# Kernel tuning notes

Measured on AMD Instinct MI355X. Metric: run time of the kernel, lower is better.

## Reference

```python
import jax, jax.numpy as jnp
import numpy as np

LN_EPS = 1e-3  # keras LayerNormalization default epsilon

def setup_inputs() -> dict:
    key = jax.random.key(0)
    ks = jax.random.split(key, 8)
    B, T, N, F_in, F_out, S = 4, 4, 65536, 16, 32, 8
    E = 589824  # ~9 edges per node (8-neighbor grid + self loop)
    return {
        "water": jax.random.normal(ks[0], (B, T, N, F_in), jnp.float32),
        "static": jax.random.uniform(ks[1], (B, T, N, S), jnp.float32),
        "adj_rows": jax.random.randint(ks[2], (E,), 0, N, jnp.int32),
        "adj_cols": jax.random.randint(ks[3], (E,), 0, N, jnp.int32),
        "adj_vals": jax.random.uniform(ks[4], (E,), jnp.float32),
        "W_feat": (jax.random.normal(ks[5], (F_in, F_out), jnp.float32) * 0.1),
        "b_feat": jnp.zeros((F_out,), jnp.float32),
        "Wg1": (jax.random.normal(ks[6], (3, 1), jnp.float32) * 0.1),
        "bg1": jnp.zeros((1,), jnp.float32),
        "Wg2": (jax.random.normal(ks[7], (S - 3, 1), jnp.float32) * 0.1),
        "bg2": jnp.zeros((1,), jnp.float32),
        "ln_gamma": jnp.ones((F_out,), jnp.float32),
        "ln_beta": jnp.zeros((F_out,), jnp.float32),
        "min_gate": jnp.float32(0.1),
    }


def reference(water, static, adj_rows, adj_cols, adj_vals,
              W_feat, b_feat, Wg1, bg1, Wg2, bg2, ln_gamma, ln_beta, min_gate):
    B, T, N, F_in = water.shape
    # gated feature scaling: gate in (0,1], per (b,t,n)
    gate = jax.nn.sigmoid(static[..., :3] @ Wg1 + bg1) * jax.nn.sigmoid(static[..., 3:] @ Wg2 + bg2)
    gate = jnp.maximum(gate, min_gate)  # [B,T,N,1]
    x = (water * gate).reshape(B * T, N, F_in)
    # SpMM shared across all F_in channels and all B*T slices:
    # out[bt,n,f] = sum_{edges (n<-m)} adj_vals * x[bt,m,f]
    xs = x.transpose(1, 0, 2)                       # [N, BT, F]
    msg = adj_vals[:, None, None] * xs[adj_cols]    # [E, BT, F]
    agg = jax.ops.segment_sum(msg, adj_rows, num_segments=N)  # [N, BT, F]
    h = agg.transpose(1, 0, 2)                      # [BT, N, F]
    out = h @ W_feat + b_feat                       # [BT, N, F_out]
    out = out.reshape(B, T, N, -1)
    # layer norm over channel axis (keras default axis=-1)
    mu = out.mean(-1, keepdims=True)
    var = out.var(-1, keepdims=True)
    out = (out - mu) * jax.lax.rsqrt(var + LN_EPS) * ln_gamma + ln_beta
    # dropout is identity at inference
    return out
```

## Files before the change

### kernel.cpp

```cpp
#include <hip/hip_runtime.h>

#define BT   16
#define FIN  16
#define FOUT 32
#define CAP  32

typedef float    f32x4 __attribute__((ext_vector_type(4)));
typedef _Float16 f16x4 __attribute__((ext_vector_type(4)));
typedef _Float16 f16x8 __attribute__((ext_vector_type(8)));
typedef unsigned int u32;


__global__ __launch_bounds__(256) void zero_kernel(int4* __restrict__ p, int n4) {
    int i = blockIdx.x * 256 + threadIdx.x;
    if (i < n4) p[i] = make_int4(0, 0, 0, 0);
}


__global__ __launch_bounds__(256) void scatter_gate_kernel(
        const int* __restrict__ rows, const int* __restrict__ cols,
        const float* __restrict__ vals,
        int* __restrict__ cur, u32* __restrict__ edge_s, int E, int eb,
        const float* __restrict__ water,
        const float* __restrict__ st,
        const float* __restrict__ Wg1, const float* __restrict__ bg1,
        const float* __restrict__ Wg2, const float* __restrict__ bg2,
        const float* __restrict__ min_gate,
        _Float16* __restrict__ x, int N) {
    if (blockIdx.x < (unsigned)eb) {
        int i0 = (blockIdx.x * 256 + threadIdx.x) * 4;
        if (i0 + 4 <= E) {
            int4   r4 = *(const int4*)  (rows + i0);
            int4   c4 = *(const int4*)  (cols + i0);
            f32x4  v4 = *(const f32x4*) (vals + i0);
#pragma unroll
            for (int k = 0; k < 4; ++k) {
                int r = (&r4.x)[k];
                int pos = atomicAdd(&cur[r], 1);
                unsigned short vh = __builtin_bit_cast(unsigned short, (_Float16)v4[k]);
                if (pos < CAP)
                    edge_s[(size_t)r * CAP + pos] = ((u32)vh << 16) | (u32)(&c4.x)[k];
            }
        } else {
            for (int e = i0; e < E; ++e) {
                int r = rows[e];
                int pos = atomicAdd(&cur[r], 1);
                unsigned short vh = __builtin_bit_cast(unsigned short, (_Float16)vals[e]);
                if (pos < CAP)
                    edge_s[(size_t)r * CAP + pos] = ((u32)vh << 16) | (u32)cols[e];
            }
        }
    } else {
        int g  = blockIdx.x - eb;
        int n  = g * 16 + (threadIdx.x & 15);
        int bt = threadIdx.x >> 4;

        const f32x4* sp = (const f32x4*)(st + ((size_t)bt * N + n) * 8);
        f32x4 s0 = sp[0];
        f32x4 s1 = sp[1];
        float g1 = s0.x * Wg1[0] + s0.y * Wg1[1] + s0.z * Wg1[2] + bg1[0];
        float g2 = s0.w * Wg2[0] + s1.x * Wg2[1] + s1.y * Wg2[2] + s1.z * Wg2[3] + s1.w * Wg2[4] + bg2[0];
        g1 = 1.f / (1.f + __expf(-g1));
        g2 = 1.f / (1.f + __expf(-g2));
        float gate = fmaxf(g1 * g2, min_gate[0]);

        const f32x4* wp = (const f32x4*)(water + ((size_t)bt * N + n) * FIN);
        f16x8 h0, h1;
#pragma unroll
        for (int k = 0; k < 4; ++k) {
            f32x4 w = wp[k];
            w *= gate;
            f16x8& h = (k < 2) ? h0 : h1;
            int b = (k & 1) * 4;
            h[b + 0] = (_Float16)w.x; h[b + 1] = (_Float16)w.y;
            h[b + 2] = (_Float16)w.z; h[b + 3] = (_Float16)w.w;
        }
        f16x8* xp = (f16x8*)(x + ((size_t)n * BT + bt) * FIN);
        xp[0] = h0;
        xp[1] = h1;
    }
}


#define GATH16(i)                                                                \
    u32 p##i = ebase[base + i];                                                  \
    f16x4 g##i = xv[(size_t)(p##i & 0xffffu) * 64 + l];

#define FMA16(i)                                                                 \
    do {                                                                         \
        u32 hv = (base + i < cnt) ? (p##i >> 16) : 0u;          \
        float v = (float)__builtin_bit_cast(_Float16, (unsigned short)hv);       \
        acc.x += v * (float)g##i[0];                                             \
        acc.y += v * (float)g##i[1];                                             \
        acc.z += v * (float)g##i[2];                                             \
        acc.w += v * (float)g##i[3];                                             \
    } while (0)

#define BATCH16                                                                  \
    GATH16(0)  GATH16(1)  GATH16(2)  GATH16(3)                                   \
    GATH16(4)  GATH16(5)  GATH16(6)  GATH16(7)                                   \
    GATH16(8)  GATH16(9)  GATH16(10) GATH16(11)                                  \
    GATH16(12) GATH16(13) GATH16(14) GATH16(15)                                  \
    FMA16(0);  FMA16(1);  FMA16(2);  FMA16(3);                                   \
    FMA16(4);  FMA16(5);  FMA16(6);  FMA16(7);                                   \
    FMA16(8);  FMA16(9);  FMA16(10); FMA16(11);                                  \
    FMA16(12); FMA16(13); FMA16(14); FMA16(15);

__global__ __launch_bounds__(256) void spmm_ln_kernel(
        const _Float16* __restrict__ x,
        const int* __restrict__ cur,
        const u32* __restrict__ edge_s,
        const float* __restrict__ W,
        const float* __restrict__ bvec,
        const float* __restrict__ gamma,
        const float* __restrict__ beta,
        float* __restrict__ out, int N) {
    __shared__ float Wsh[FIN][FOUT];
    __shared__ float psh[3][FOUT];

    int t = threadIdx.x;
    Wsh[t >> 5][t & 31]       = W[t];
    Wsh[(t >> 5) + 8][t & 31] = W[t + 256];
    if (t < 32)       psh[0][t]      = bvec[t];
    else if (t < 64)  psh[1][t - 32] = gamma[t - 32];
    else if (t < 96)  psh[2][t - 64] = beta[t - 64];
    __syncthreads();

    int l = t & 63;
    int n = __builtin_amdgcn_readfirstlane(blockIdx.x * 4 + (t >> 6));
    int cnt = __builtin_amdgcn_readfirstlane(cur[n]);
    cnt = (cnt < CAP) ? cnt : CAP;
    const u32* ebase = edge_s + (size_t)n * CAP;
    const f16x4* xv = (const f16x4*)x;

    f32x4 acc = {0.f, 0.f, 0.f, 0.f};
    {
        int base = 0;
        BATCH16
    }
    if (cnt > 16) {
        int base = 16;
        BATCH16
    }

    int d = l & 3;
    float o[8];
#pragma unroll
    for (int jj = 0; jj < 8; ++jj) o[jj] = psh[0][d * 8 + jj];
#pragma unroll
    for (int q = 0; q < 4; ++q) {
        float hq[4];
        hq[0] = __shfl(acc.x, q, 4);
        hq[1] = __shfl(acc.y, q, 4);
        hq[2] = __shfl(acc.z, q, 4);
        hq[3] = __shfl(acc.w, q, 4);
#pragma unroll
        for (int m = 0; m < 4; ++m) {
            float hk = hq[m];
#pragma unroll
            for (int jj = 0; jj < 8; ++jj)
                o[jj] += hk * Wsh[q * 4 + m][d * 8 + jj];
        }
    }

    float s = 0.f, sq = 0.f;
#pragma unroll
    for (int jj = 0; jj < 8; ++jj) { s += o[jj]; sq += o[jj] * o[jj]; }
    s  += __shfl_xor(s,  1, 4);  sq += __shfl_xor(sq, 1, 4);
    s  += __shfl_xor(s,  2, 4);  sq += __shfl_xor(sq, 2, 4);
    float mu  = s * (1.f / 32.f);
    float var = sq * (1.f / 32.f) - mu * mu;
    float inv = rsqrtf(var + 1e-3f);

    f32x4 r0, r1;
#pragma unroll
    for (int jj = 0; jj < 8; ++jj) {
        float val = (o[jj] - mu) * inv * psh[1][d * 8 + jj] + psh[2][d * 8 + jj];
        if (jj < 4) r0[jj] = val;
        else        r1[jj - 4] = val;
    }
    int bt = l >> 2;
    f32x4* op = (f32x4*)(out + (size_t)bt * N * FOUT + (size_t)n * FOUT + d * 8);
    op[0] = r0;
    op[1] = r1;
}


extern "C" void kernel_launch(void* const* d_in, const int* in_sizes, int n_in,
                              void* d_out, int out_size, void* d_ws, size_t ws_size,
                              hipStream_t stream) {
    const float* water    = (const float*)d_in[0];
    const float* st       = (const float*)d_in[1];
    const int*   adj_rows = (const int*)  d_in[2];
    const int*   adj_cols = (const int*)  d_in[3];
    const float* adj_vals = (const float*)d_in[4];
    const float* W_feat   = (const float*)d_in[5];
    const float* b_feat   = (const float*)d_in[6];
    const float* Wg1      = (const float*)d_in[7];
    const float* bg1      = (const float*)d_in[8];
    const float* Wg2      = (const float*)d_in[9];
    const float* bg2      = (const float*)d_in[10];
    const float* ln_gamma = (const float*)d_in[11];
    const float* ln_beta  = (const float*)d_in[12];
    const float* min_gate = (const float*)d_in[13];
    float* out = (float*)d_out;

    int N = in_sizes[0] / (BT * FIN);
    int E = in_sizes[2];

    char* ws = (char*)d_ws;
    size_t off = 0;
    auto alloc = [&](size_t bytes) -> void* {
        off = (off + 255) & ~(size_t)255;
        void* p = ws + off;
        off += bytes;
        return p;
    };
    int*      cur    = (int*)     alloc((size_t)N * sizeof(int));
    u32*      edge_s = (u32*)     alloc((size_t)N * CAP * sizeof(u32));
    _Float16* x      = (_Float16*)alloc((size_t)N * BT * FIN * sizeof(_Float16));

    int eb = (E + 1023) / 1024;
    int gb = N / 16;

    zero_kernel<<<N / 1024, 256, 0, stream>>>((int4*)cur, N / 4);
    scatter_gate_kernel<<<eb + gb, 256, 0, stream>>>(
        adj_rows, adj_cols, adj_vals, cur, edge_s, E, eb,
        water, st, Wg1, bg1, Wg2, bg2, min_gate, x, N);
    spmm_ln_kernel<<<N / 4, 256, 0, stream>>>(
        x, cur, edge_s, W_feat, b_feat, ln_gamma, ln_beta, out, N);
}
```

Before: 129.4 us.

## Skip padded gather batches by edge count and coalesce output stores via LDS

The first 16-edge gather batch is now entered through a fallthrough switch on the edge count rounded up to a multiple of four, so nodes with fewer edges skip the unused index and feature loads instead of always issuing all 16. The output is staged in shared memory (padded to avoid bank conflicts) and written back so that each block's four nodes form contiguous 512-byte runs per bt slice, replacing scattered 32-byte writes. This adds an extra __syncthreads and LDS traffic per block, and the variable-length switch may introduce some divergence-free branching overhead.

New measurement: 130.3 us. About the same (+0.7%).

```diff
diff --git a/kernel.cpp b/kernel.cpp
--- a/kernel.cpp
+++ b/kernel.cpp
@@ -82,29 +82,22 @@
 }
 
 
-#define GATH16(i)                                                                \
-    u32 p##i = ebase[base + i];                                                  \
-    f16x4 g##i = xv[(size_t)(p##i & 0xffffu) * 64 + l];
-
-#define FMA16(i)                                                                 \
-    do {                                                                         \
-        u32 hv = (base + i < cnt) ? (p##i >> 16) : 0u;          \
+#define GA(i)  p##i = ebase[i];      g##i = xv[(size_t)(p##i & 0xffffu) * 64 + l];
+#define GB(i)  p##i = ebase[16 + i]; g##i = xv[(size_t)(p##i & 0xffffu) * 64 + l];
+#define FM(i)                                                                    \
+    {                                                                            \
+        u32 hv = (i < cnt) ? (p##i >> 16) : 0u;                                  \
         float v = (float)__builtin_bit_cast(_Float16, (unsigned short)hv);       \
-        acc.x += v * (float)g##i[0];                                             \
-        acc.y += v * (float)g##i[1];                                             \
-        acc.z += v * (float)g##i[2];                                             \
-        acc.w += v * (float)g##i[3];                                             \
-    } while (0)
-
-#define BATCH16                                                                  \
-    GATH16(0)  GATH16(1)  GATH16(2)  GATH16(3)                                   \
-    GATH16(4)  GATH16(5)  GATH16(6)  GATH16(7)                                   \
-    GATH16(8)  GATH16(9)  GATH16(10) GATH16(11)                                  \
-    GATH16(12) GATH16(13) GATH16(14) GATH16(15)                                  \
-    FMA16(0);  FMA16(1);  FMA16(2);  FMA16(3);                                   \
-    FMA16(4);  FMA16(5);  FMA16(6);  FMA16(7);                                   \
-    FMA16(8);  FMA16(9);  FMA16(10); FMA16(11);                                  \
-    FMA16(12); FMA16(13); FMA16(14); FMA16(15);
+        acc.x += v * (float)g##i[0];  acc.y += v * (float)g##i[1];               \
+        acc.z += v * (float)g##i[2];  acc.w += v * (float)g##i[3];               \
+    }
+#define FB(i)                                                                    \
+    {                                                                            \
+        u32 hv = (16 + i < cnt) ? (p##i >> 16) : 0u;                             \
+        float v = (float)__builtin_bit_cast(_Float16, (unsigned short)hv);       \
+        acc.x += v * (float)g##i[0];  acc.y += v * (float)g##i[1];               \
+        acc.z += v * (float)g##i[2];  acc.w += v * (float)g##i[3];               \
+    }
 
 __global__ __launch_bounds__(256) void spmm_ln_kernel(
         const _Float16* __restrict__ x,
@@ -117,6 +110,7 @@
         float* __restrict__ out, int N) {
     __shared__ float Wsh[FIN][FOUT];
     __shared__ float psh[3][FOUT];
+    __shared__ f32x4 osh[4][BT][9];
 
     int t = threadIdx.x;
     Wsh[t >> 5][t & 31]       = W[t];
@@ -126,21 +120,39 @@
     else if (t < 96)  psh[2][t - 64] = beta[t - 64];
     __syncthreads();
 
-    int l = t & 63;
-    int n = __builtin_amdgcn_readfirstlane(blockIdx.x * 4 + (t >> 6));
+    int l  = t & 63;
+    int wv = t >> 6;
+    int n = __builtin_amdgcn_readfirstlane(blockIdx.x * 4 + wv);
     int cnt = __builtin_amdgcn_readfirstlane(cur[n]);
     cnt = (cnt < CAP) ? cnt : CAP;
+    int pcnt = (cnt + 3) & ~3;
+    int k4 = pcnt >> 2; k4 = (k4 < 4) ? k4 : 4;
     const u32* ebase = edge_s + (size_t)n * CAP;
     const f16x4* xv = (const f16x4*)x;
 
+    u32 p0,p1,p2,p3,p4,p5,p6,p7,p8,p9,p10,p11,p12,p13,p14,p15;
+    f16x4 g0,g1,g2,g3,g4,g5,g6,g7,g8,g9,g10,g11,g12,g13,g14,g15;
     f32x4 acc = {0.f, 0.f, 0.f, 0.f};
-    {
-        int base = 0;
-        BATCH16
+
+    switch (k4) {
+        case 4: GA(12) GA(13) GA(14) GA(15)
+        case 3: GA(8)  GA(9)  GA(10) GA(11)
+        case 2: GA(4)  GA(5)  GA(6)  GA(7)
+        case 1: GA(0)  GA(1)  GA(2)  GA(3)  break;
+        default: break;
+    }
+    switch (k4) {
+        case 4: FM(12) FM(13) FM(14) FM(15)
+        case 3: FM(8)  FM(9)  FM(10) FM(11)
+        case 2: FM(4)  FM(5)  FM(6)  FM(7)
+        case 1: FM(0)  FM(1)  FM(2)  FM(3)  break;
+        default: break;
     }
     if (cnt > 16) {
-        int base = 16;
-        BATCH16
+        GB(0) GB(1) GB(2) GB(3) GB(4) GB(5) GB(6) GB(7)
+        GB(8) GB(9) GB(10) GB(11) GB(12) GB(13) GB(14) GB(15)
+        FB(0) FB(1) FB(2) FB(3) FB(4) FB(5) FB(6) FB(7)
+        FB(8) FB(9) FB(10) FB(11) FB(12) FB(13) FB(14) FB(15)
     }
 
     int d = l & 3;
@@ -180,9 +192,21 @@
         else        r1[jj - 4] = val;
     }
     int bt = l >> 2;
-    f32x4* op = (f32x4*)(out + (size_t)bt * N * FOUT + (size_t)n * FOUT + d * 8);
-    op[0] = r0;
-    op[1] = r1;
+    osh[wv][bt][d * 2]     = r0;
+    osh[wv][bt][d * 2 + 1] = r1;
+    __syncthreads();
+
+    int n0 = blockIdx.x * 4;
+#pragma unroll
+    for (int ps = 0; ps < 2; ++ps) {
+        int idx = ps * 256 + t;
+        int bt2 = idx >> 5;
+        int q2  = idx & 31;
+        int j   = q2 >> 3;
+        int v   = q2 & 7;
+        f32x4 r = osh[j][bt2][v];
+        *(f32x4*)(out + (size_t)bt2 * N * FOUT + (size_t)(n0 + j) * FOUT + v * 4) = r;
+    }
 }
 
 
```
